# Performance work log

Hardware: AMD Instinct MI355X
Metric: run time of the kernel (lower is better)

Reference implementation:

```python
import jax, jax.numpy as jnp
import numpy as np

N = 50000        # num nodes
E = 800000       # num edges
F_IN = 128
H1 = 256
H2 = 256
C = 64


def _sage_conv(x, edge_index, W_l, b_l, W_r):
    """PyG SAGEConv (mean aggr): lin_l(mean over in-neighbors of x_j) + lin_r(x)."""
    src = edge_index[0]
    dst = edge_index[1]
    n = x.shape[0]
    # gather messages [E, d] then segment-mean into [N, d]
    agg = jax.ops.segment_sum(x[src], dst, num_segments=n)
    cnt = jax.ops.segment_sum(jnp.ones((edge_index.shape[1],), x.dtype), dst, num_segments=n)
    mean = agg / jnp.maximum(cnt, 1.0)[:, None]
    return mean @ W_l + b_l + x @ W_r


def setup_inputs() -> dict:
    key = jax.random.key(0)
    ks = jax.random.split(key, 10)
    x = jax.random.normal(ks[0], (N, F_IN), dtype=jnp.float32)
    edge_index = jax.random.randint(ks[1], (2, E), 0, N, dtype=jnp.int64)
    s1 = 1.0 / np.sqrt(F_IN)
    s2 = 1.0 / np.sqrt(H1)
    s3 = 1.0 / np.sqrt(H2)
    return {
        "x": x,
        "edge_index": edge_index,
        "W1_l": jax.random.uniform(ks[2], (F_IN, H1), jnp.float32, -s1, s1),
        "b1": jnp.zeros((H1,), jnp.float32),
        "W1_r": jax.random.uniform(ks[3], (F_IN, H1), jnp.float32, -s1, s1),
        "W2_l": jax.random.uniform(ks[4], (H1, H2), jnp.float32, -s2, s2),
        "b2": jnp.zeros((H2,), jnp.float32),
        "W2_r": jax.random.uniform(ks[5], (H1, H2), jnp.float32, -s2, s2),
        "Wc": jax.random.uniform(ks[6], (H2, C), jnp.float32, -s3, s3),
        "bc": jax.random.uniform(ks[7], (C,), jnp.float32, -s3, s3),
    }


def reference(x, edge_index, W1_l, b1, W1_r, W2_l, b2, W2_r, Wc, bc):
    # inference mode: dropout is identity
    h = jax.nn.relu(_sage_conv(x, edge_index, W1_l, b1, W1_r))
    h = jax.nn.relu(_sage_conv(h, edge_index, W2_l, b2, W2_r))
    return h @ Wc + bc
```

## Files before the change

### kernel.cpp

```cpp
#include <hip/hip_runtime.h>
#include <hip/hip_bf16.h>


#define F_IN 128
#define H1_DIM 256
#define H2_DIM 256
#define C_DIM 64

typedef __attribute__((ext_vector_type(8))) short bf16x8;
typedef __attribute__((ext_vector_type(8))) unsigned short u16x8;
typedef __attribute__((ext_vector_type(4))) float f32x4;

__device__ __forceinline__ unsigned short f2bf(float f) {
    unsigned u = __builtin_bit_cast(unsigned, f);
    u = (u + 0x7FFFu + ((u >> 16) & 1u)) >> 16;
    return (unsigned short)u;
}
__device__ __forceinline__ float bf2f(unsigned short h) {
    return __builtin_bit_cast(float, (unsigned)h << 16);
}

__global__ void k_detect(const unsigned int* __restrict__ ei, int* __restrict__ flag) {
    if (blockIdx.x == 0 && threadIdx.x == 0) {
        int is64 = 1;
        for (int i = 1; i < 256; i += 2) {
            if (ei[i] != 0u) { is64 = 0; break; }
        }
        *flag = is64;
    }
}

__device__ __forceinline__ int ei_at(const void* ei, const int* flag, long long idx) {
    return (*flag) ? (int)((const long long*)ei)[idx] : ((const int*)ei)[idx];
}

__global__ void k_degree(const void* __restrict__ ei, const int* __restrict__ flag,
                         int* __restrict__ cnt, int E) {
    int i = blockIdx.x * blockDim.x + threadIdx.x;
    if (i >= E) return;
    atomicAdd(&cnt[ei_at(ei, flag, (long long)E + i)], 1);
}

__global__ void k_scan1(const int* __restrict__ cnt, int* __restrict__ rowptr,
                        int* __restrict__ bsum, int n) {
    __shared__ int s[256];
    int i = blockIdx.x * 256 + threadIdx.x;
    int v = (i < n) ? cnt[i] : 0;
    s[threadIdx.x] = v;
    __syncthreads();
    for (int off = 1; off < 256; off <<= 1) {
        int t = (threadIdx.x >= off) ? s[threadIdx.x - off] : 0;
        __syncthreads();
        s[threadIdx.x] += t;
        __syncthreads();
    }
    if (i < n) rowptr[i] = s[threadIdx.x] - v;
    if (threadIdx.x == 255) bsum[blockIdx.x] = s[255];
}

__global__ void k_scan2(const int* __restrict__ bsum, int* __restrict__ boff, int nb) {
    __shared__ int s[1024];
    int t = threadIdx.x;
    int v = (t < nb) ? bsum[t] : 0;
    s[t] = v;
    __syncthreads();
    for (int off = 1; off < 1024; off <<= 1) {
        int u = (t >= off) ? s[t - off] : 0;
        __syncthreads();
        s[t] += u;
        __syncthreads();
    }
    if (t < nb) boff[t] = s[t] - v;
}

__global__ void k_scan3(int* __restrict__ rowptr, const int* __restrict__ boff,
                        int n, int total) {
    int i = blockIdx.x * 256 + threadIdx.x;
    if (i < n) rowptr[i] += boff[i >> 8];
    if (i == 0) rowptr[n] = total;
}

__global__ void k_scatter(const void* __restrict__ ei, const int* __restrict__ flag,
                          const int* __restrict__ rowptr, int* __restrict__ pos,
                          int* __restrict__ col, int E) {
    int i = blockIdx.x * blockDim.x + threadIdx.x;
    if (i >= E) return;
    int s = ei_at(ei, flag, i);
    int d = ei_at(ei, flag, (long long)E + i);
    int p = atomicAdd(&pos[d], 1);
    col[rowptr[d] + p] = s;
}

__global__ void k_prep_x(const float* __restrict__ x, unsigned short* __restrict__ hi,
                         unsigned short* __restrict__ lo, int n4) {
    int i = blockIdx.x * 256 + threadIdx.x;
    if (i >= n4) return;
    float4 v = ((const float4*)x)[i];
    ushort4 h, l;
    h.x = f2bf(v.x); l.x = f2bf(v.x - bf2f(h.x));
    h.y = f2bf(v.y); l.y = f2bf(v.y - bf2f(h.y));
    h.z = f2bf(v.z); l.z = f2bf(v.z - bf2f(h.z));
    h.w = f2bf(v.w); l.w = f2bf(v.w - bf2f(h.w));
    ((ushort4*)hi)[i] = h;
    ((ushort4*)lo)[i] = l;
}

struct WPrep {
    const float* W;
    unsigned short* hiT;
    unsigned short* loT;
    int K;
    int NN;
};

__global__ void k_prep_w(WPrep w0, WPrep w1, WPrep w2, WPrep w3, WPrep w4) {
    WPrep wp;
    switch (blockIdx.y) {
        case 0: wp = w0; break;
        case 1: wp = w1; break;
        case 2: wp = w2; break;
        case 3: wp = w3; break;
        default: wp = w4; break;
    }
    int total = wp.K * wp.NN;
    for (int i = blockIdx.x * 256 + threadIdx.x; i < total; i += gridDim.x * 256) {
        int k = i / wp.NN, n = i % wp.NN;
        float v = wp.W[i];
        unsigned short h = f2bf(v);
        wp.hiT[(size_t)n * wp.K + k] = h;
        wp.loT[(size_t)n * wp.K + k] = f2bf(v - bf2f(h));
    }
}

__global__ void k_agg1(const unsigned short* __restrict__ xhi,
                       const int* __restrict__ rowptr, const int* __restrict__ col,
                       unsigned short* __restrict__ mhi, unsigned short* __restrict__ mlo,
                       int n) {
    int w = blockIdx.x * 4 + (threadIdx.x >> 6);
    int lane = threadIdx.x & 63;
    if (w >= n) return;
    int q = lane >> 4;
    int ch = (lane & 15) * 8;
    int beg = rowptr[w], end = rowptr[w + 1];
    float inv = 1.0f / fmaxf((float)(end - beg), 1.0f);

    float a[8];
#pragma unroll
    for (int c = 0; c < 8; ++c) a[c] = 0.f;

    int j = beg + q;
    for (; j + 4 < end; j += 8) {
        int c0 = col[j], c1 = col[j + 4];
        u16x8 r0 = *(const u16x8*)(xhi + (size_t)c0 * 128 + ch);
        u16x8 r1 = *(const u16x8*)(xhi + (size_t)c1 * 128 + ch);
#pragma unroll
        for (int c = 0; c < 8; ++c) a[c] += bf2f(r0[c]) + bf2f(r1[c]);
    }
    if (j < end) {
        u16x8 r0 = *(const u16x8*)(xhi + (size_t)col[j] * 128 + ch);
#pragma unroll
        for (int c = 0; c < 8; ++c) a[c] += bf2f(r0[c]);
    }

#pragma unroll
    for (int c = 0; c < 8; ++c) a[c] += __shfl_xor(a[c], 16);
#pragma unroll
    for (int c = 0; c < 8; ++c) a[c] += __shfl_xor(a[c], 32);

    if (q < 2) {
        u16x8 o;
#pragma unroll
        for (int c = 0; c < 8; ++c) {
            float m = a[c] * inv;
            unsigned short h = f2bf(m);
            o[c] = (q == 0) ? h : f2bf(m - bf2f(h));
        }
        unsigned short* dst = (q == 0) ? mhi : mlo;
        *(u16x8*)(dst + (size_t)w * 128 + ch) = o;
    }
}

__global__ void k_agg2(const unsigned short* __restrict__ hhi,
                       const int* __restrict__ rowptr, const int* __restrict__ col,
                       unsigned short* __restrict__ mhi, unsigned short* __restrict__ mlo,
                       int n) {
    int w = blockIdx.x * 4 + (threadIdx.x >> 6);
    int lane = threadIdx.x & 63;
    if (w >= n) return;
    int h = lane >> 5;
    int ch = (lane & 31) * 8;
    int beg = rowptr[w], end = rowptr[w + 1];
    float inv = 1.0f / fmaxf((float)(end - beg), 1.0f);

    float a[8];
#pragma unroll
    for (int c = 0; c < 8; ++c) a[c] = 0.f;

    int j = beg + h;
    for (; j + 2 < end; j += 4) {
        int c0 = col[j], c1 = col[j + 2];
        u16x8 r0 = *(const u16x8*)(hhi + (size_t)c0 * 256 + ch);
        u16x8 r1 = *(const u16x8*)(hhi + (size_t)c1 * 256 + ch);
#pragma unroll
        for (int c = 0; c < 8; ++c) a[c] += bf2f(r0[c]) + bf2f(r1[c]);
    }
    if (j < end) {
        u16x8 r0 = *(const u16x8*)(hhi + (size_t)col[j] * 256 + ch);
#pragma unroll
        for (int c = 0; c < 8; ++c) a[c] += bf2f(r0[c]);
    }

#pragma unroll
    for (int c = 0; c < 8; ++c) a[c] += __shfl_xor(a[c], 32);

    u16x8 o;
#pragma unroll
    for (int c = 0; c < 8; ++c) {
        float m = a[c] * inv;
        unsigned short hh = f2bf(m);
        o[c] = (h == 0) ? hh : f2bf(m - bf2f(hh));
    }
    unsigned short* dst = (h == 0) ? mhi : mlo;
    *(u16x8*)(dst + (size_t)w * 256 + ch) = o;
}

struct Segs {
    const unsigned short* a[6];
    const unsigned short* b[6];
};

template <int BN, int NSEG, int KS, bool RELU, int OUTMODE>
__global__ void k_mfma_gemm(Segs segs, const float* __restrict__ bias,
                            float* __restrict__ Cf, unsigned short* __restrict__ Chi,
                            unsigned short* __restrict__ Clo, int M, int NN) {
    constexpr int BM = 128;
    constexpr int WN = BN / 2;
    constexpr int FM = 4;
    constexpr int FN = WN / 16;
    constexpr int ACH = 16;
    constexpr int BCH = BN / 8;

    __shared__ unsigned short sA[BM * 64];
    __shared__ unsigned short sB[BN * 64];

    const int tid = threadIdx.x;
    const int lane = tid & 63;
    const int wid = tid >> 6;
    const int wr = wid >> 1, wc = wid & 1;

    const int nbn = NN / BN;
    const int bm = blockIdx.x / nbn;
    const int bn = blockIdx.x % nbn;
    const int row0 = bm * BM;
    const int col0 = bn * BN;

    f32x4 acc[FM][FN];
#pragma unroll
    for (int m = 0; m < FM; ++m)
#pragma unroll
        for (int n = 0; n < FN; ++n) acc[m][n] = (f32x4){0.f, 0.f, 0.f, 0.f};

    const int st_r = lane >> 3;
    const int st_k = (lane & 7) * 8;

    for (int seg = 0; seg < NSEG; ++seg) {
        const unsigned short* Ag = segs.a[seg];
        const unsigned short* Bg = segs.b[seg];
        for (int k0 = 0; k0 < KS; k0 += 64) {
            for (int c = wid; c < ACH; c += 4) {
                int gr = row0 + c * 8 + st_r;
                if (gr >= M) gr = 0;
                const unsigned short* gp = Ag + (size_t)gr * KS + k0 + st_k;
                __builtin_amdgcn_global_load_lds(
                    (const __attribute__((address_space(1))) unsigned int*)gp,
                    (__attribute__((address_space(3))) unsigned int*)(sA + c * 512),
                    16, 0, 0);
            }
            for (int c = wid; c < BCH; c += 4) {
                int gn = col0 + c * 8 + st_r;
                const unsigned short* gp = Bg + (size_t)gn * KS + k0 + st_k;
                __builtin_amdgcn_global_load_lds(
                    (const __attribute__((address_space(1))) unsigned int*)gp,
                    (__attribute__((address_space(3))) unsigned int*)(sB + c * 512),
                    16, 0, 0);
            }
            __syncthreads();

#pragma unroll
            for (int ks = 0; ks < 2; ++ks) {
                bf16x8 af[FM], bfr[FN];
#pragma unroll
                for (int m = 0; m < FM; ++m) {
                    int rb = wr * 64 + m * 16 + (lane & 15);
                    af[m] = *(const bf16x8*)(sA + (size_t)rb * 64 + ks * 32 + (lane >> 4) * 8);
                }
#pragma unroll
                for (int n = 0; n < FN; ++n) {
                    int cb = wc * WN + n * 16 + (lane & 15);
                    bfr[n] = *(const bf16x8*)(sB + (size_t)cb * 64 + ks * 32 + (lane >> 4) * 8);
                }
#pragma unroll
                for (int m = 0; m < FM; ++m)
#pragma unroll
                    for (int n = 0; n < FN; ++n)
                        acc[m][n] = __builtin_amdgcn_mfma_f32_16x16x32_bf16(
                            af[m], bfr[n], acc[m][n], 0, 0, 0);
            }
            __syncthreads();
        }
    }

#pragma unroll
    for (int m = 0; m < FM; ++m) {
#pragma unroll
        for (int n = 0; n < FN; ++n) {
            int col = col0 + wc * WN + n * 16 + (lane & 15);
            float bb = bias[col];
#pragma unroll
            for (int r = 0; r < 4; ++r) {
                int row = row0 + wr * 64 + m * 16 + (lane >> 4) * 4 + r;
                if (row < M) {
                    float t = acc[m][n][r] + bb;
                    if (RELU) t = fmaxf(t, 0.f);
                    if (OUTMODE == 0) {
                        Cf[(size_t)row * NN + col] = t;
                    } else {
                        unsigned short hi = f2bf(t);
                        float lo = t - bf2f(hi);
                        Chi[(size_t)row * NN + col] = hi;
                        Clo[(size_t)row * NN + col] = f2bf(lo);
                    }
                }
            }
        }
    }
}

extern "C" void kernel_launch(void* const* d_in, const int* in_sizes, int n_in,
                              void* d_out, int out_size, void* d_ws, size_t ws_size,
                              hipStream_t stream) {
    const float* x   = (const float*)d_in[0];
    const void*  ei  = d_in[1];
    const float* W1l = (const float*)d_in[2];
    const float* b1  = (const float*)d_in[3];
    const float* W1r = (const float*)d_in[4];
    const float* W2l = (const float*)d_in[5];
    const float* b2  = (const float*)d_in[6];
    const float* W2r = (const float*)d_in[7];
    const float* Wc  = (const float*)d_in[8];
    const float* bc  = (const float*)d_in[9];
    float* out = (float*)d_out;

    const int N = in_sizes[0] / F_IN;
    const int E = in_sizes[1] / 2;

    typedef unsigned short u16;

    char* w = (char*)d_ws;
    size_t off = 0;
    auto carve = [&](size_t bytes) -> char* {
        char* p = w + off;
        off = (off + bytes + 255) & ~(size_t)255;
        return p;
    };
    int* cnt    = (int*)carve((size_t)N * 4);
    int* pos    = (int*)carve((size_t)N * 4);
    int* rowptr = (int*)carve((size_t)(N + 1) * 4);
    int* bsum   = (int*)carve(1024 * 4);
    int* boff   = (int*)carve(1024 * 4);
    int* flag   = (int*)carve(256);
    int* col    = (int*)carve((size_t)E * 4);

    u16* xhi    = (u16*)carve((size_t)N * F_IN * 2);
    u16* xlo    = (u16*)carve((size_t)N * F_IN * 2);
    u16* agghi  = (u16*)carve((size_t)N * 256 * 2);
    u16* agglo  = (u16*)carve((size_t)N * 256 * 2);
    u16* h1hi   = (u16*)carve((size_t)N * 256 * 2);
    u16* h1lo   = (u16*)carve((size_t)N * 256 * 2);
    u16* h2lo   = (u16*)carve((size_t)N * 256 * 2);
    u16* h2hi   = xhi;

    u16* w1l_hi = (u16*)carve((size_t)F_IN * H1_DIM * 2);
    u16* w1l_lo = (u16*)carve((size_t)F_IN * H1_DIM * 2);
    u16* w1r_hi = (u16*)carve((size_t)F_IN * H1_DIM * 2);
    u16* w1r_lo = (u16*)carve((size_t)F_IN * H1_DIM * 2);
    u16* w2l_hi = (u16*)carve((size_t)H1_DIM * H2_DIM * 2);
    u16* w2l_lo = (u16*)carve((size_t)H1_DIM * H2_DIM * 2);
    u16* w2r_hi = (u16*)carve((size_t)H1_DIM * H2_DIM * 2);
    u16* w2r_lo = (u16*)carve((size_t)H1_DIM * H2_DIM * 2);
    u16* wc_hi  = (u16*)carve((size_t)H2_DIM * C_DIM * 2);
    u16* wc_lo  = (u16*)carve((size_t)H2_DIM * C_DIM * 2);
    (void)ws_size;

    hipMemsetAsync(cnt, 0, (char*)rowptr - (char*)cnt, stream);

    k_detect<<<1, 64, 0, stream>>>((const unsigned int*)ei, flag);
    k_degree<<<(E + 255) / 256, 256, 0, stream>>>(ei, flag, cnt, E);
    int nb = (N + 255) / 256;
    k_scan1<<<nb, 256, 0, stream>>>(cnt, rowptr, bsum, N);
    k_scan2<<<1, 1024, 0, stream>>>(bsum, boff, nb);
    k_scan3<<<nb, 256, 0, stream>>>(rowptr, boff, N, E);
    k_scatter<<<(E + 255) / 256, 256, 0, stream>>>(ei, flag, rowptr, pos, col, E);

    k_prep_x<<<((N * F_IN / 4) + 255) / 256, 256, 0, stream>>>(x, xhi, xlo, N * F_IN / 4);
    {
        WPrep w0{W1l, w1l_hi, w1l_lo, F_IN, H1_DIM};
        WPrep w1{W1r, w1r_hi, w1r_lo, F_IN, H1_DIM};
        WPrep w2{W2l, w2l_hi, w2l_lo, H1_DIM, H2_DIM};
        WPrep w3{W2r, w2r_hi, w2r_lo, H1_DIM, H2_DIM};
        WPrep w4{Wc, wc_hi, wc_lo, H2_DIM, C_DIM};
        dim3 g(64, 5);
        k_prep_w<<<g, 256, 0, stream>>>(w0, w1, w2, w3, w4);
    }

    const int nbm = (N + 127) / 128;

    k_agg1<<<(N + 3) / 4, 256, 0, stream>>>(xhi, rowptr, col, agghi, agglo, N);
    {
        Segs s;
        s.a[0] = agghi; s.b[0] = w1l_hi;
        s.a[1] = agglo; s.b[1] = w1l_hi;
        s.a[2] = agghi; s.b[2] = w1l_lo;
        s.a[3] = xhi;   s.b[3] = w1r_hi;
        s.a[4] = xlo;   s.b[4] = w1r_hi;
        s.a[5] = xhi;   s.b[5] = w1r_lo;
        k_mfma_gemm<128, 6, 128, true, 1><<<nbm * (H1_DIM / 128), 256, 0, stream>>>(
            s, b1, nullptr, h1hi, h1lo, N, H1_DIM);
    }

    k_agg2<<<(N + 3) / 4, 256, 0, stream>>>(h1hi, rowptr, col, agghi, agglo, N);
    {
        Segs s;
        s.a[0] = agghi; s.b[0] = w2l_hi;
        s.a[1] = agglo; s.b[1] = w2l_hi;
        s.a[2] = agghi; s.b[2] = w2l_lo;
        s.a[3] = h1hi;  s.b[3] = w2r_hi;
        s.a[4] = h1lo;  s.b[4] = w2r_hi;
        s.a[5] = h1hi;  s.b[5] = w2r_lo;
        k_mfma_gemm<128, 6, 256, true, 1><<<nbm * (H2_DIM / 128), 256, 0, stream>>>(
            s, b2, nullptr, h2hi, h2lo, N, H2_DIM);
    }

    {
        Segs s;
        s.a[0] = h2hi; s.b[0] = wc_hi;
        s.a[1] = h2lo; s.b[1] = wc_hi;
        s.a[2] = h2hi; s.b[2] = wc_lo;
        s.a[3] = nullptr; s.b[3] = nullptr;
        s.a[4] = nullptr; s.b[4] = nullptr;
        s.a[5] = nullptr; s.b[5] = nullptr;
        k_mfma_gemm<64, 3, 256, false, 0><<<nbm, 256, 0, stream>>>(
            s, bc, out, nullptr, nullptr, N, C_DIM);
    }
}
```

Measured before the change: 415.3 us.

## Share A tiles across hi/lo weights, widen GEMM tile to full N, swizzle LDS

The split-bf16 GEMM now loads each activation tile once and multiplies it against both the hi and lo weight tiles. This cuts the segment passes from six to four, so fewer A loads are issued. The hidden-layer GEMMs use a 128x256 tile with 8 waves, so each row block reads its activations only once instead of once per 128-column half. LDS staging also gets an XOR swizzle to reduce bank conflicts on fragment reads. In exchange, per-block LDS and register use grow, which may lower occupancy.

```diff
diff --git a/kernel.cpp b/kernel.cpp
--- a/kernel.cpp
+++ b/kernel.cpp
@@ -224,33 +224,38 @@
     *(u16x8*)(dst + (size_t)w * 256 + ch) = o;
 }
 
-struct Segs {
-    const unsigned short* a[6];
-    const unsigned short* b[6];
+struct Loads {
+    const unsigned short* a[4];
+    const unsigned short* b0[4];
+    const unsigned short* b1[4];
 };
 
-template <int BN, int NSEG, int KS, bool RELU, int OUTMODE>
-__global__ void k_mfma_gemm(Segs segs, const float* __restrict__ bias,
-                            float* __restrict__ Cf, unsigned short* __restrict__ Chi,
-                            unsigned short* __restrict__ Clo, int M, int NN) {
+template <int BN, int NLOAD, int KS, bool RELU, int OUTMODE, int WAVES>
+__global__ __launch_bounds__(WAVES * 64, 2) void k_mfma_gemm(
+    Loads L, const float* __restrict__ bias,
+    float* __restrict__ Cf, unsigned short* __restrict__ Chi,
+    unsigned short* __restrict__ Clo, int M, int NN) {
     constexpr int BM = 128;
-    constexpr int WN = BN / 2;
-    constexpr int FM = 4;
+    constexpr int WCN = (BN >= 256) ? 4 : 2;
+    constexpr int WRN = WAVES / WCN;
+    constexpr int WM = BM / WRN;
+    constexpr int WN = BN / WCN;
+    constexpr int FM = WM / 16;
     constexpr int FN = WN / 16;
     constexpr int ACH = 16;
     constexpr int BCH = BN / 8;
 
     __shared__ unsigned short sA[BM * 64];
-    __shared__ unsigned short sB[BN * 64];
+    __shared__ unsigned short sB[2][BN * 64];
 
     const int tid = threadIdx.x;
     const int lane = tid & 63;
     const int wid = tid >> 6;
-    const int wr = wid >> 1, wc = wid & 1;
+    const int wr = wid / WCN, wc = wid % WCN;
 
     const int nbn = NN / BN;
-    const int bm = blockIdx.x / nbn;
-    const int bn = blockIdx.x % nbn;
+    const int bm = (nbn == 1) ? blockIdx.x : blockIdx.x / nbn;
+    const int bn = (nbn == 1) ? 0 : blockIdx.x % nbn;
     const int row0 = bm * BM;
     const int col0 = bn * BN;
 
@@ -260,14 +265,21 @@
 #pragma unroll
         for (int n = 0; n < FN; ++n) acc[m][n] = (f32x4){0.f, 0.f, 0.f, 0.f};
 
+    const int l7 = lane & 7;
+    const int l15 = lane & 15;
+    const int q = lane >> 4;
     const int st_r = lane >> 3;
-    const int st_k = (lane & 7) * 8;
-
-    for (int seg = 0; seg < NSEG; ++seg) {
-        const unsigned short* Ag = segs.a[seg];
-        const unsigned short* Bg = segs.b[seg];
+    const int st_k = 8 * (l7 ^ st_r);
+
+    for (int ld = 0; ld < NLOAD; ++ld) {
+        const unsigned short* Ag = L.a[ld];
+        const unsigned short* B0 = L.b0[ld];
+        const unsigned short* B1 = L.b1[ld];
+        const bool dual = (B1 != nullptr);
+
         for (int k0 = 0; k0 < KS; k0 += 64) {
-            for (int c = wid; c < ACH; c += 4) {
+#pragma unroll
+            for (int c = wid; c < ACH; c += WAVES) {
                 int gr = row0 + c * 8 + st_r;
                 if (gr >= M) gr = 0;
                 const unsigned short* gp = Ag + (size_t)gr * KS + k0 + st_k;
@@ -276,35 +288,63 @@
                     (__attribute__((address_space(3))) unsigned int*)(sA + c * 512),
                     16, 0, 0);
             }
-            for (int c = wid; c < BCH; c += 4) {
+#pragma unroll
+            for (int c = wid; c < BCH; c += WAVES) {
                 int gn = col0 + c * 8 + st_r;
-                const unsigned short* gp = Bg + (size_t)gn * KS + k0 + st_k;
+                const unsigned short* gp = B0 + (size_t)gn * KS + k0 + st_k;
                 __builtin_amdgcn_global_load_lds(
                     (const __attribute__((address_space(1))) unsigned int*)gp,
-                    (__attribute__((address_space(3))) unsigned int*)(sB + c * 512),
+                    (__attribute__((address_space(3))) unsigned int*)(sB[0] + c * 512),
                     16, 0, 0);
             }
+            if (dual) {
+#pragma unroll
+                for (int c = wid; c < BCH; c += WAVES) {
+                    int gn = col0 + c * 8 + st_r;
+                    const unsigned short* gp = B1 + (size_t)gn * KS + k0 + st_k;
+                    __builtin_amdgcn_global_load_lds(
+                        (const __attribute__((address_space(1))) unsigned int*)gp,
+                        (__attribute__((address_space(3))) unsigned int*)(sB[1] + c * 512),
+                        16, 0, 0);
+                }
+            }
             __syncthreads();
 
 #pragma unroll
             for (int ks = 0; ks < 2; ++ks) {
-                bf16x8 af[FM], bfr[FN];
+                const int sidx = 8 * ((q + 4 * ks) ^ l7);
+                bf16x8 af[FM], b0f[FN], b1f[FN];
 #pragma unroll
                 for (int m = 0; m < FM; ++m) {
-                    int rb = wr * 64 + m * 16 + (lane & 15);
-                    af[m] = *(const bf16x8*)(sA + (size_t)rb * 64 + ks * 32 + (lane >> 4) * 8);
+                    int rb = wr * WM + m * 16 + l15;
+                    af[m] = *(const bf16x8*)(sA + (size_t)rb * 64 + sidx);
                 }
 #pragma unroll
                 for (int n = 0; n < FN; ++n) {
-                    int cb = wc * WN + n * 16 + (lane & 15);
-                    bfr[n] = *(const bf16x8*)(sB + (size_t)cb * 64 + ks * 32 + (lane >> 4) * 8);
+                    int cb = wc * WN + n * 16 + l15;
+                    b0f[n] = *(const bf16x8*)(sB[0] + (size_t)cb * 64 + sidx);
+                }
+                if (dual) {
+#pragma unroll
+                    for (int n = 0; n < FN; ++n) {
+                        int cb = wc * WN + n * 16 + l15;
+                        b1f[n] = *(const bf16x8*)(sB[1] + (size_t)cb * 64 + sidx);
+                    }
                 }
 #pragma unroll
                 for (int m = 0; m < FM; ++m)
 #pragma unroll
                     for (int n = 0; n < FN; ++n)
                         acc[m][n] = __builtin_amdgcn_mfma_f32_16x16x32_bf16(
-                            af[m], bfr[n], acc[m][n], 0, 0, 0);
+                            af[m], b0f[n], acc[m][n], 0, 0, 0);
+                if (dual) {
+#pragma unroll
+                    for (int m = 0; m < FM; ++m)
+#pragma unroll
+                        for (int n = 0; n < FN; ++n)
+                            acc[m][n] = __builtin_amdgcn_mfma_f32_16x16x32_bf16(
+                                af[m], b1f[n], acc[m][n], 0, 0, 0);
+                }
             }
             __syncthreads();
         }
@@ -314,11 +354,11 @@
     for (int m = 0; m < FM; ++m) {
 #pragma unroll
         for (int n = 0; n < FN; ++n) {
-            int col = col0 + wc * WN + n * 16 + (lane & 15);
+            int col = col0 + wc * WN + n * 16 + l15;
             float bb = bias[col];
 #pragma unroll
             for (int r = 0; r < 4; ++r) {
-                int row = row0 + wr * 64 + m * 16 + (lane >> 4) * 4 + r;
+                int row = row0 + wr * WM + m * 16 + q * 4 + r;
                 if (row < M) {
                     float t = acc[m][n][r] + bb;
                     if (RELU) t = fmaxf(t, 0.f);
@@ -417,39 +457,33 @@
 
     k_agg1<<<(N + 3) / 4, 256, 0, stream>>>(xhi, rowptr, col, agghi, agglo, N);
     {
-        Segs s;
-        s.a[0] = agghi; s.b[0] = w1l_hi;
-        s.a[1] = agglo; s.b[1] = w1l_hi;
-        s.a[2] = agghi; s.b[2] = w1l_lo;
-        s.a[3] = xhi;   s.b[3] = w1r_hi;
-        s.a[4] = xlo;   s.b[4] = w1r_hi;
-        s.a[5] = xhi;   s.b[5] = w1r_lo;
-        k_mfma_gemm<128, 6, 128, true, 1><<<nbm * (H1_DIM / 128), 256, 0, stream>>>(
-            s, b1, nullptr, h1hi, h1lo, N, H1_DIM);
+        Loads L;
+        L.a[0] = agghi; L.b0[0] = w1l_hi; L.b1[0] = w1l_lo;
+        L.a[1] = agglo; L.b0[1] = w1l_hi; L.b1[1] = nullptr;
+        L.a[2] = xhi;   L.b0[2] = w1r_hi; L.b1[2] = w1r_lo;
+        L.a[3] = xlo;   L.b0[3] = w1r_hi; L.b1[3] = nullptr;
+        k_mfma_gemm<256, 4, 128, true, 1, 8><<<nbm, 512, 0, stream>>>(
+            L, b1, nullptr, h1hi, h1lo, N, H1_DIM);
     }
 
     k_agg2<<<(N + 3) / 4, 256, 0, stream>>>(h1hi, rowptr, col, agghi, agglo, N);
     {
-        Segs s;
-        s.a[0] = agghi; s.b[0] = w2l_hi;
-        s.a[1] = agglo; s.b[1] = w2l_hi;
-        s.a[2] = agghi; s.b[2] = w2l_lo;
-        s.a[3] = h1hi;  s.b[3] = w2r_hi;
-        s.a[4] = h1lo;  s.b[4] = w2r_hi;
-        s.a[5] = h1hi;  s.b[5] = w2r_lo;
-        k_mfma_gemm<128, 6, 256, true, 1><<<nbm * (H2_DIM / 128), 256, 0, stream>>>(
-            s, b2, nullptr, h2hi, h2lo, N, H2_DIM);
+        Loads L;
+        L.a[0] = agghi; L.b0[0] = w2l_hi; L.b1[0] = w2l_lo;
+        L.a[1] = agglo; L.b0[1] = w2l_hi; L.b1[1] = nullptr;
+        L.a[2] = h1hi;  L.b0[2] = w2r_hi; L.b1[2] = w2r_lo;
+        L.a[3] = h1lo;  L.b0[3] = w2r_hi; L.b1[3] = nullptr;
+        k_mfma_gemm<256, 4, 256, true, 1, 8><<<nbm, 512, 0, stream>>>(
+            L, b2, nullptr, h2hi, h2lo, N, H2_DIM);
     }
 
     {
-        Segs s;
-        s.a[0] = h2hi; s.b[0] = wc_hi;
-        s.a[1] = h2lo; s.b[1] = wc_hi;
-        s.a[2] = h2hi; s.b[2] = wc_lo;
-        s.a[3] = nullptr; s.b[3] = nullptr;
-        s.a[4] = nullptr; s.b[4] = nullptr;
-        s.a[5] = nullptr; s.b[5] = nullptr;
-        k_mfma_gemm<64, 3, 256, false, 0><<<nbm, 256, 0, stream>>>(
-            s, bc, out, nullptr, nullptr, N, C_DIM);
-    }
-}
+        Loads L;
+        L.a[0] = h2hi; L.b0[0] = wc_hi; L.b1[0] = wc_lo;
+        L.a[1] = h2lo; L.b0[1] = wc_hi; L.b1[1] = nullptr;
+        L.a[2] = nullptr; L.b0[2] = nullptr; L.b1[2] = nullptr;
+        L.a[3] = nullptr; L.b0[3] = nullptr; L.b1[3] = nullptr;
+        k_mfma_gemm<64, 2, 256, false, 0, 4><<<nbm, 256, 0, stream>>>(
+            L, bc, out, nullptr, nullptr, N, C_DIM);
+    }
+}
```

New measurement: 418.2 us. About the same (+0.7%).
